# Kernel optimization log

Hardware: AMD Instinct MI355X
Metric: run time of the kernel (lower is better)

Reference implementation:

```python
import jax, jax.numpy as jnp
import numpy as np

B, S, D, H = 2, 2048, 1024, 16
DK = D // H


def setup_inputs() -> dict:
    key = jax.random.key(0)
    ks = jax.random.split(key, 12)
    sc = 0.02
    return {
        "q": jax.random.normal(ks[0], (B, S, D), jnp.float32),
        "k": jax.random.normal(ks[1], (B, S, D), jnp.float32),
        "v": jax.random.normal(ks[2], (B, S, D), jnp.float32),
        "Wq": jax.random.normal(ks[3], (D, D), jnp.float32) * sc,
        "bq": jnp.zeros((D,), jnp.float32),
        "Wk": jax.random.normal(ks[4], (D, D), jnp.float32) * sc,
        "bk": jnp.zeros((D,), jnp.float32),
        "Wv": jax.random.normal(ks[5], (D, D), jnp.float32) * sc,
        "bv": jnp.zeros((D,), jnp.float32),
        "Wo": jax.random.normal(ks[6], (D, D), jnp.float32) * sc,
        "bo": jnp.zeros((D,), jnp.float32),
        "mask": jnp.ones((1, 1, S, S), jnp.int32),
    }


def reference(q, k, v, Wq, bq, Wk, bk, Wv, bv, Wo, bo, mask):
    # Linear projections (torch Linear: x @ W.T + b)
    query = q @ Wq.T + bq  # [B, S, D]
    key_ = k @ Wk.T + bk
    value = v @ Wv.T + bv
    # split heads -> [B, H, S, DK]
    def split(x):
        return x.reshape(B, S, H, DK).transpose(0, 2, 1, 3)
    query, key_, value = split(query), split(key_), split(value)
    scores = jnp.einsum("bhqd,bhkd->bhqk", query, key_) / jnp.sqrt(jnp.float32(DK))
    scores = jnp.where(mask == 0, jnp.float32(-1e9), scores)
    attn = jax.nn.softmax(scores, axis=-1)  # dropout=0.0 -> identity
    out = jnp.einsum("bhqk,bhkd->bhqd", attn, value)  # [B, H, S, DK]
    out = out.transpose(0, 2, 1, 3).reshape(B, S, D)
    return out @ Wo.T + bo
```

## Files before the change

### kernel.cpp

```cpp
#include <hip/hip_runtime.h>

typedef unsigned short u16;
typedef float f32x4 __attribute__((ext_vector_type(4)));
typedef __bf16 bf16x8 __attribute__((ext_vector_type(8)));
typedef short s16x8 __attribute__((ext_vector_type(8)));
typedef short s16x4 __attribute__((ext_vector_type(4)));

#define QSCALE 0.18033688011112042f

__device__ __forceinline__ u16 f2bf(float f) {
    unsigned int u = __builtin_bit_cast(unsigned int, f);
    u += 0x7fffu + ((u >> 16) & 1u);
    return (u16)(u >> 16);
}

__device__ __forceinline__ f32x4 mfma16(s16x8 a, s16x8 b, f32x4 c) {
    return __builtin_amdgcn_mfma_f32_16x16x32_bf16(
        __builtin_bit_cast(bf16x8, a), __builtin_bit_cast(bf16x8, b), c, 0, 0, 0);
}

__device__ __forceinline__ void cp16(const u16* g, u16* l) {
    __builtin_amdgcn_global_load_lds(
        (const __attribute__((address_space(1))) unsigned int*)g,
        (__attribute__((address_space(3))) unsigned int*)l, 16, 0, 0);
}

__global__ __launch_bounds__(256) void k_cvt(
    const float* q, const float* k, const float* v,
    const float* Wq, const float* Wk, const float* Wv, const float* Wo,
    u16* qb, u16* kb, u16* vb, u16* Wqb, u16* Wkb, u16* Wvb, u16* Wob) {
    const float* src;
    u16* dst;
    int count;
    switch (blockIdx.y) {
        case 0: src = q;  dst = qb;  count = 4194304; break;
        case 1: src = k;  dst = kb;  count = 4194304; break;
        case 2: src = v;  dst = vb;  count = 4194304; break;
        case 3: src = Wq; dst = Wqb; count = 1048576; break;
        case 4: src = Wk; dst = Wkb; count = 1048576; break;
        case 5: src = Wv; dst = Wvb; count = 1048576; break;
        default: src = Wo; dst = Wob; count = 1048576; break;
    }
    const int idx = (blockIdx.x * 256 + threadIdx.x) * 8;
    if (idx >= count) return;
    const f32x4 f0 = *(const f32x4*)(src + idx);
    const f32x4 f1 = *(const f32x4*)(src + idx + 4);
    s16x8 o;
#pragma unroll
    for (int i = 0; i < 4; i++) o[i] = (short)f2bf(f0[i]);
#pragma unroll
    for (int i = 0; i < 4; i++) o[4 + i] = (short)f2bf(f1[i]);
    *(s16x8*)(dst + idx) = o;
}

__device__ __forceinline__ void gemm_dev(const u16* __restrict__ A,
                                         const u16* __restrict__ W,
                                         const float* __restrict__ bias,
                                         u16* __restrict__ dstb,
                                         float* __restrict__ dstf,
                                         int mode, float scale) {
    constexpr int K = 1024;
    __shared__ u16 As[128 * 64];
    __shared__ u16 Bs[128 * 64];
    const int tid = threadIdx.x;
    const int wid = tid >> 6, lane = tid & 63;
    const int ln = lane & 15, qd = lane >> 4;
    const int wm = wid >> 1, wn = wid & 1;
    const int m0 = blockIdx.y * 128, n0 = blockIdx.x * 128;
    const int lrow = lane >> 3, lcol = (lane & 7) * 8;

    f32x4 acc[4][4] = {};

    for (int k0 = 0; k0 < K; k0 += 64) {
        __syncthreads();
#pragma unroll
        for (int c = 0; c < 4; c++) {
            const int ch = wid * 4 + c;
            cp16(A + (m0 + ch * 8 + lrow) * K + k0 + lcol, &As[ch * 512]);
            cp16(W + (n0 + ch * 8 + lrow) * K + k0 + lcol, &Bs[ch * 512]);
        }
        __syncthreads();
#pragma unroll
        for (int kk = 0; kk < 64; kk += 32) {
            s16x8 af[4], bf[4];
#pragma unroll
            for (int t = 0; t < 4; t++) {
                af[t] = *(const s16x8*)&As[(wm * 64 + t * 16 + ln) * 64 + kk + qd * 8];
                bf[t] = *(const s16x8*)&Bs[(wn * 64 + t * 16 + ln) * 64 + kk + qd * 8];
            }
#pragma unroll
            for (int tm = 0; tm < 4; tm++)
#pragma unroll
                for (int tn = 0; tn < 4; tn++)
                    acc[tm][tn] = mfma16(af[tm], bf[tn], acc[tm][tn]);
        }
    }

#pragma unroll
    for (int tn = 0; tn < 4; tn++) {
        const int gn = n0 + wn * 64 + tn * 16 + ln;
        const float bv = bias[gn];
        const int h = gn >> 6, dk = gn & 63;
#pragma unroll
        for (int tm = 0; tm < 4; tm++) {
            const int gmb = m0 + wm * 64 + tm * 16 + qd * 4;
            const f32x4 a = acc[tm][tn];
            if (mode == 0) {
                const int b = gmb >> 11;
#pragma unroll
                for (int r = 0; r < 4; r++) {
                    const int s = (gmb + r) & 2047;
                    dstb[(((b * 16 + h) * 2048) + s) * 64 + dk] =
                        f2bf((a[r] + bv) * scale);
                }
            } else if (mode == 2) {
                const int b = gmb >> 11, s = gmb & 2047;
                s16x4 pk;
#pragma unroll
                for (int r = 0; r < 4; r++) pk[r] = (short)f2bf(a[r] + bv);
                *(s16x4*)&dstb[(((b * 16 + h) * 64) + dk) * 2048 + s] = pk;
            } else {
#pragma unroll
                for (int r = 0; r < 4; r++)
                    dstf[(gmb + r) * 1024 + gn] = a[r] + bv;
            }
        }
    }
}

__global__ __launch_bounds__(256, 2) void k_gemm_qkv(
    const u16* qb, const u16* kb, const u16* vb,
    const u16* Wqb, const u16* Wkb, const u16* Wvb,
    const float* bq, const float* bk, const float* bv,
    u16* Qw, u16* Kw, u16* Vt) {
    const int z = blockIdx.z;
    const u16* A = (z == 0) ? qb : (z == 1) ? kb : vb;
    const u16* W = (z == 0) ? Wqb : (z == 1) ? Wkb : Wvb;
    const float* bi = (z == 0) ? bq : (z == 1) ? bk : bv;
    u16* dst = (z == 0) ? Qw : (z == 1) ? Kw : Vt;
    const int mode = (z == 2) ? 2 : 0;
    const float scale = (z == 0) ? QSCALE : 1.0f;
    gemm_dev(A, W, bi, dst, nullptr, mode, scale);
}

__global__ __launch_bounds__(256, 2) void k_gemm_o(const u16* A, const u16* W,
                                                   const float* bias, float* out) {
    gemm_dev(A, W, bias, nullptr, out, 1, 1.0f);
}

__global__ __launch_bounds__(256, 2) void k_attn(const u16* __restrict__ Qw,
                                                 const u16* __restrict__ Kw,
                                                 const u16* __restrict__ Vt,
                                                 u16* __restrict__ AO) {
    __shared__ u16 Ks[128 * 64];
    __shared__ u16 Vs[64 * 128];

    const int i = blockIdx.x;
    const int xcd = i & 7, qq = i >> 3;
    const int bh = xcd * 4 + (qq >> 4);
    const int qblk = qq & 15;
    const int tid = threadIdx.x;
    const int wid = tid >> 6, lane = tid & 63;
    const int ln = lane & 15, qd = lane >> 4;
    const int q0 = qblk * 128 + wid * 32;

    const u16* Qp = Qw + (bh * 2048 + q0 + ln) * 64 + qd * 8;
    const s16x8 qA0 = *(const s16x8*)Qp;
    const s16x8 qA1 = *(const s16x8*)(Qp + 32);
    const s16x8 qB0 = *(const s16x8*)(Qp + 16 * 64);
    const s16x8 qB1 = *(const s16x8*)(Qp + 16 * 64 + 32);

    int Kgoff[4], Vgoff[4];
#pragma unroll
    for (int c = 0; c < 4; c++) {
        const int ch = wid * 4 + c;
        {
            const int kl = ch * 8 + (lane >> 3);
            const int slot = lane & 7;
            const int cK = (slot - 2 * (kl & 7) - (kl >> 3)) & 7;
            Kgoff[c] = (bh * 2048 + kl) * 64 + cK * 8;
        }
        {
            const int d = ch * 4 + (lane >> 4);
            const int slot = lane & 15;
            const int cV = (slot - d) & 15;
            Vgoff[c] = (bh * 64 + d) * 2048 + cV * 8;
        }
    }

    const int kf0 = (ln >> 2) * 8 + (ln & 3);
    const int rotbase = 2 * (ln & 3) + (ln >> 2);

    f32x4 oA[4] = {}, oB[4] = {};
    float lsA = 0.0f, lsB = 0.0f;
    const f32x4 zero = {};

    for (int kb = 0; kb < 2048; kb += 128) {
        __syncthreads();
#pragma unroll
        for (int c = 0; c < 4; c++) {
            cp16(Kw + Kgoff[c] + kb * 64, &Ks[(wid * 4 + c) * 512]);
            cp16(Vt + Vgoff[c] + kb,      &Vs[(wid * 4 + c) * 512]);
        }
        __syncthreads();
#pragma unroll
        for (int sc = 0; sc < 4; sc++) {
            const int rot = (rotbase + sc * 4) & 7;
            const int s0 = (qd + rot) & 7;
            const int kbase = (sc * 32 + kf0) * 64;
            const s16x8 k00 = *(const s16x8*)&Ks[kbase + s0 * 8];
            const s16x8 k01 = *(const s16x8*)&Ks[kbase + (s0 ^ 4) * 8];
            const s16x8 k10 = *(const s16x8*)&Ks[kbase + 256 + s0 * 8];
            const s16x8 k11 = *(const s16x8*)&Ks[kbase + 256 + (s0 ^ 4) * 8];

            f32x4 cA0 = mfma16(k00, qA0, zero); cA0 = mfma16(k01, qA1, cA0);
            f32x4 cA1 = mfma16(k10, qA0, zero); cA1 = mfma16(k11, qA1, cA1);
            f32x4 cB0 = mfma16(k00, qB0, zero); cB0 = mfma16(k01, qB1, cB0);
            f32x4 cB1 = mfma16(k10, qB0, zero); cB1 = mfma16(k11, qB1, cB1);

            bf16x8 pA, pB;
#pragma unroll
            for (int j = 0; j < 4; j++) {
                const float p = __builtin_amdgcn_exp2f(cA0[j]);
                lsA += p; pA[j] = (__bf16)p;
            }
#pragma unroll
            for (int j = 0; j < 4; j++) {
                const float p = __builtin_amdgcn_exp2f(cA1[j]);
                lsA += p; pA[4 + j] = (__bf16)p;
            }
#pragma unroll
            for (int j = 0; j < 4; j++) {
                const float p = __builtin_amdgcn_exp2f(cB0[j]);
                lsB += p; pB[j] = (__bf16)p;
            }
#pragma unroll
            for (int j = 0; j < 4; j++) {
                const float p = __builtin_amdgcn_exp2f(cB1[j]);
                lsB += p; pB[4 + j] = (__bf16)p;
            }
            const s16x8 pAs = __builtin_bit_cast(s16x8, pA);
            const s16x8 pBs = __builtin_bit_cast(s16x8, pB);

            const int vslot = ((sc * 4 + qd + ln) & 15) * 8;
#pragma unroll
            for (int t = 0; t < 4; t++) {
                const s16x8 vf = *(const s16x8*)&Vs[(t * 16 + ln) * 128 + vslot];
                oA[t] = mfma16(vf, pAs, oA[t]);
                oB[t] = mfma16(vf, pBs, oB[t]);
            }
        }
    }

    lsA += __shfl_xor(lsA, 16, 64);
    lsA += __shfl_xor(lsA, 32, 64);
    lsB += __shfl_xor(lsB, 16, 64);
    lsB += __shfl_xor(lsB, 32, 64);
    const float rlA = 1.0f / lsA;
    const float rlB = 1.0f / lsB;

    const int b = bh >> 4, h = bh & 15;
    u16* outA = AO + (b * 2048 + q0 + ln) * 1024 + h * 64;
    u16* outB = outA + 16 * 1024;
#pragma unroll
    for (int t = 0; t < 4; t++)
#pragma unroll
        for (int r = 0; r < 4; r++) {
            const int d = t * 16 + qd * 4 + r;
            outA[d] = f2bf(oA[t][r] * rlA);
            outB[d] = f2bf(oB[t][r] * rlB);
        }
}

extern "C" void kernel_launch(void* const* d_in, const int* in_sizes, int n_in,
                              void* d_out, int out_size, void* d_ws, size_t ws_size,
                              hipStream_t stream) {
    const float* q  = (const float*)d_in[0];
    const float* k  = (const float*)d_in[1];
    const float* v  = (const float*)d_in[2];
    const float* Wq = (const float*)d_in[3];
    const float* bq = (const float*)d_in[4];
    const float* Wk = (const float*)d_in[5];
    const float* bk = (const float*)d_in[6];
    const float* Wv = (const float*)d_in[7];
    const float* bv = (const float*)d_in[8];
    const float* Wo = (const float*)d_in[9];
    const float* bo = (const float*)d_in[10];

    u16* ws = (u16*)d_ws;
    u16* qb  = ws;
    u16* kb  = ws + 4194304;
    u16* vb  = ws + 8388608;
    u16* Wqb = ws + 12582912;
    u16* Wkb = ws + 13631488;
    u16* Wvb = ws + 14680064;
    u16* Wob = ws + 15728640;
    u16* Qw  = ws + 16777216;
    u16* Kw  = ws + 20971520;
    u16* Vt  = ws + 25165824;
    u16* AO  = qb;

    k_cvt<<<dim3(2048, 7), dim3(256), 0, stream>>>(q, k, v, Wq, Wk, Wv, Wo,
                                                   qb, kb, vb, Wqb, Wkb, Wvb, Wob);
    k_gemm_qkv<<<dim3(8, 32, 3), dim3(256), 0, stream>>>(qb, kb, vb, Wqb, Wkb, Wvb,
                                                         bq, bk, bv, Qw, Kw, Vt);
    k_attn<<<dim3(512), dim3(256), 0, stream>>>(Qw, Kw, Vt, AO);
    k_gemm_o<<<dim3(8, 32, 1), dim3(256), 0, stream>>>(AO, Wob, bo, (float*)d_out);
}
```

Measured before the change: 236.6 us.

## Fuse fp32 activation conversion into QKV GEMM and restructure attention wave split

Drops the separate fp32-to-bf16 conversion of q/k/v. The QKV GEMM now loads fp32 activations straight into LDS and converts them to bf16 when building fragments, which removes a full write and re-read of the activations. The attention kernel is reorganised so each wave covers 64 queries over half the keys per tile, reusing each K/V fragment across four query fragments. The two key-halves are then reduced through LDS and written out as coalesced 16-byte stores. In exchange the GEMM doubles its LDS footprint for A tiles, and attention adds extra LDS reduction passes and synchronisation plus higher register pressure.

```diff
diff --git a/kernel.cpp b/kernel.cpp
--- a/kernel.cpp
+++ b/kernel.cpp
@@ -19,30 +19,24 @@
         __builtin_bit_cast(bf16x8, a), __builtin_bit_cast(bf16x8, b), c, 0, 0, 0);
 }
 
-__device__ __forceinline__ void cp16(const u16* g, u16* l) {
+__device__ __forceinline__ void cp16(const void* g, void* l) {
     __builtin_amdgcn_global_load_lds(
         (const __attribute__((address_space(1))) unsigned int*)g,
         (__attribute__((address_space(3))) unsigned int*)l, 16, 0, 0);
 }
 
-__global__ __launch_bounds__(256) void k_cvt(
-    const float* q, const float* k, const float* v,
+__global__ __launch_bounds__(256) void k_cvt_w(
     const float* Wq, const float* Wk, const float* Wv, const float* Wo,
-    u16* qb, u16* kb, u16* vb, u16* Wqb, u16* Wkb, u16* Wvb, u16* Wob) {
+    u16* Wqb, u16* Wkb, u16* Wvb, u16* Wob) {
     const float* src;
     u16* dst;
-    int count;
     switch (blockIdx.y) {
-        case 0: src = q;  dst = qb;  count = 4194304; break;
-        case 1: src = k;  dst = kb;  count = 4194304; break;
-        case 2: src = v;  dst = vb;  count = 4194304; break;
-        case 3: src = Wq; dst = Wqb; count = 1048576; break;
-        case 4: src = Wk; dst = Wkb; count = 1048576; break;
-        case 5: src = Wv; dst = Wvb; count = 1048576; break;
-        default: src = Wo; dst = Wob; count = 1048576; break;
+        case 0: src = Wq; dst = Wqb; break;
+        case 1: src = Wk; dst = Wkb; break;
+        case 2: src = Wv; dst = Wvb; break;
+        default: src = Wo; dst = Wob; break;
     }
     const int idx = (blockIdx.x * 256 + threadIdx.x) * 8;
-    if (idx >= count) return;
     const f32x4 f0 = *(const f32x4*)(src + idx);
     const f32x4 f1 = *(const f32x4*)(src + idx + 4);
     s16x8 o;
@@ -53,15 +47,95 @@
     *(s16x8*)(dst + idx) = o;
 }
 
-__device__ __forceinline__ void gemm_dev(const u16* __restrict__ A,
-                                         const u16* __restrict__ W,
-                                         const float* __restrict__ bias,
-                                         u16* __restrict__ dstb,
-                                         float* __restrict__ dstf,
-                                         int mode, float scale) {
-    constexpr int K = 1024;
-    __shared__ u16 As[128 * 64];
-    __shared__ u16 Bs[128 * 64];
+__global__ __launch_bounds__(256, 2) void k_gemm_qkv(
+    const float* q, const float* k, const float* v,
+    const u16* Wqb, const u16* Wkb, const u16* Wvb,
+    const float* bq, const float* bk, const float* bv,
+    u16* Qw, u16* Kw, u16* Vt) {
+    __shared__ __align__(16) float Asf[128 * 64];
+    __shared__ __align__(16) u16 Ws[128 * 64];
+    const int z = blockIdx.z;
+    const float* A = (z == 0) ? q : (z == 1) ? k : v;
+    const u16* Wb = (z == 0) ? Wqb : (z == 1) ? Wkb : Wvb;
+    const float* bias = (z == 0) ? bq : (z == 1) ? bk : bv;
+    const float scale = (z == 0) ? QSCALE : 1.0f;
+
+    const int tid = threadIdx.x;
+    const int wid = tid >> 6, lane = tid & 63;
+    const int ln = lane & 15, qd = lane >> 4;
+    const int wm = wid >> 1, wn = wid & 1;
+    const int m0 = blockIdx.y * 128, n0 = blockIdx.x * 128;
+
+    f32x4 acc[4][4] = {};
+
+    for (int k0 = 0; k0 < 1024; k0 += 64) {
+        __syncthreads();
+#pragma unroll
+        for (int c = 0; c < 8; c++) {
+            const int ch = wid * 8 + c;
+            cp16(A + (m0 + ch * 4 + (lane >> 4)) * 1024 + k0 + (lane & 15) * 4,
+                 &Asf[ch * 256]);
+        }
+#pragma unroll
+        for (int c = 0; c < 4; c++) {
+            const int ch = wid * 4 + c;
+            cp16(Wb + (n0 + ch * 8 + (lane >> 3)) * 1024 + k0 + (lane & 7) * 8,
+                 &Ws[ch * 512]);
+        }
+        __syncthreads();
+#pragma unroll
+        for (int kk = 0; kk < 64; kk += 32) {
+            s16x8 af[4], bf[4];
+#pragma unroll
+            for (int t = 0; t < 4; t++) {
+                const float* ap = &Asf[(wm * 64 + t * 16 + ln) * 64 + kk + qd * 8];
+                const f32x4 a0 = *(const f32x4*)ap;
+                const f32x4 a1 = *(const f32x4*)(ap + 4);
+                bf16x8 tmp;
+#pragma unroll
+                for (int i = 0; i < 4; i++) { tmp[i] = (__bf16)a0[i]; tmp[4 + i] = (__bf16)a1[i]; }
+                af[t] = __builtin_bit_cast(s16x8, tmp);
+                bf[t] = *(const s16x8*)&Ws[(wn * 64 + t * 16 + ln) * 64 + kk + qd * 8];
+            }
+#pragma unroll
+            for (int tm = 0; tm < 4; tm++)
+#pragma unroll
+                for (int tn = 0; tn < 4; tn++)
+                    acc[tm][tn] = mfma16(af[tm], bf[tn], acc[tm][tn]);
+        }
+    }
+
+#pragma unroll
+    for (int tn = 0; tn < 4; tn++) {
+        const int gn = n0 + wn * 64 + tn * 16 + ln;
+        const float bv2 = bias[gn];
+        const int h = gn >> 6, dk = gn & 63;
+#pragma unroll
+        for (int tm = 0; tm < 4; tm++) {
+            const int gmb = m0 + wm * 64 + tm * 16 + qd * 4;
+            const f32x4 a = acc[tm][tn];
+            const int b = gmb >> 11, s = gmb & 2047;
+            if (z != 2) {
+#pragma unroll
+                for (int r = 0; r < 4; r++)
+                    ((z == 0) ? Qw : Kw)[(((b * 16 + h) * 2048) + s + r) * 64 + dk] =
+                        f2bf((a[r] + bv2) * scale);
+            } else {
+                s16x4 pk;
+#pragma unroll
+                for (int r = 0; r < 4; r++) pk[r] = (short)f2bf(a[r] + bv2);
+                *(s16x4*)&Vt[(((b * 16 + h) * 64) + dk) * 2048 + s] = pk;
+            }
+        }
+    }
+}
+
+__global__ __launch_bounds__(256, 2) void k_gemm_o(const u16* __restrict__ A,
+                                                   const u16* __restrict__ W,
+                                                   const float* __restrict__ bias,
+                                                   float* __restrict__ out) {
+    __shared__ __align__(16) u16 As[128 * 64];
+    __shared__ __align__(16) u16 Bs[128 * 64];
     const int tid = threadIdx.x;
     const int wid = tid >> 6, lane = tid & 63;
     const int ln = lane & 15, qd = lane >> 4;
@@ -70,14 +144,13 @@
     const int lrow = lane >> 3, lcol = (lane & 7) * 8;
 
     f32x4 acc[4][4] = {};
-
-    for (int k0 = 0; k0 < K; k0 += 64) {
+    for (int k0 = 0; k0 < 1024; k0 += 64) {
         __syncthreads();
 #pragma unroll
         for (int c = 0; c < 4; c++) {
             const int ch = wid * 4 + c;
-            cp16(A + (m0 + ch * 8 + lrow) * K + k0 + lcol, &As[ch * 512]);
-            cp16(W + (n0 + ch * 8 + lrow) * K + k0 + lcol, &Bs[ch * 512]);
+            cp16(A + (m0 + ch * 8 + lrow) * 1024 + k0 + lcol, &As[ch * 512]);
+            cp16(W + (n0 + ch * 8 + lrow) * 1024 + k0 + lcol, &Bs[ch * 512]);
         }
         __syncthreads();
 #pragma unroll
@@ -95,65 +168,29 @@
                     acc[tm][tn] = mfma16(af[tm], bf[tn], acc[tm][tn]);
         }
     }
-
 #pragma unroll
     for (int tn = 0; tn < 4; tn++) {
         const int gn = n0 + wn * 64 + tn * 16 + ln;
         const float bv = bias[gn];
-        const int h = gn >> 6, dk = gn & 63;
 #pragma unroll
         for (int tm = 0; tm < 4; tm++) {
             const int gmb = m0 + wm * 64 + tm * 16 + qd * 4;
             const f32x4 a = acc[tm][tn];
-            if (mode == 0) {
-                const int b = gmb >> 11;
-#pragma unroll
-                for (int r = 0; r < 4; r++) {
-                    const int s = (gmb + r) & 2047;
-                    dstb[(((b * 16 + h) * 2048) + s) * 64 + dk] =
-                        f2bf((a[r] + bv) * scale);
-                }
-            } else if (mode == 2) {
-                const int b = gmb >> 11, s = gmb & 2047;
-                s16x4 pk;
-#pragma unroll
-                for (int r = 0; r < 4; r++) pk[r] = (short)f2bf(a[r] + bv);
-                *(s16x4*)&dstb[(((b * 16 + h) * 64) + dk) * 2048 + s] = pk;
-            } else {
-#pragma unroll
-                for (int r = 0; r < 4; r++)
-                    dstf[(gmb + r) * 1024 + gn] = a[r] + bv;
-            }
-        }
-    }
-}
-
-__global__ __launch_bounds__(256, 2) void k_gemm_qkv(
-    const u16* qb, const u16* kb, const u16* vb,
-    const u16* Wqb, const u16* Wkb, const u16* Wvb,
-    const float* bq, const float* bk, const float* bv,
-    u16* Qw, u16* Kw, u16* Vt) {
-    const int z = blockIdx.z;
-    const u16* A = (z == 0) ? qb : (z == 1) ? kb : vb;
-    const u16* W = (z == 0) ? Wqb : (z == 1) ? Wkb : Wvb;
-    const float* bi = (z == 0) ? bq : (z == 1) ? bk : bv;
-    u16* dst = (z == 0) ? Qw : (z == 1) ? Kw : Vt;
-    const int mode = (z == 2) ? 2 : 0;
-    const float scale = (z == 0) ? QSCALE : 1.0f;
-    gemm_dev(A, W, bi, dst, nullptr, mode, scale);
-}
-
-__global__ __launch_bounds__(256, 2) void k_gemm_o(const u16* A, const u16* W,
-                                                   const float* bias, float* out) {
-    gemm_dev(A, W, bias, nullptr, out, 1, 1.0f);
+#pragma unroll
+            for (int r = 0; r < 4; r++) out[(gmb + r) * 1024 + gn] = a[r] + bv;
+        }
+    }
 }
 
 __global__ __launch_bounds__(256, 2) void k_attn(const u16* __restrict__ Qw,
                                                  const u16* __restrict__ Kw,
                                                  const u16* __restrict__ Vt,
                                                  u16* __restrict__ AO) {
-    __shared__ u16 Ks[128 * 64];
-    __shared__ u16 Vs[64 * 128];
+    __shared__ __align__(16) u16 smem[16896];
+    u16* Ks = smem;
+    u16* Vs = smem + 8192;
+    float* Of = (float*)smem;
+    float* Lf = (float*)(smem + 16384);
 
     const int i = blockIdx.x;
     const int xcd = i & 7, qq = i >> 3;
@@ -162,13 +199,16 @@
     const int tid = threadIdx.x;
     const int wid = tid >> 6, lane = tid & 63;
     const int ln = lane & 15, qd = lane >> 4;
-    const int q0 = qblk * 128 + wid * 32;
-
-    const u16* Qp = Qw + (bh * 2048 + q0 + ln) * 64 + qd * 8;
-    const s16x8 qA0 = *(const s16x8*)Qp;
-    const s16x8 qA1 = *(const s16x8*)(Qp + 32);
-    const s16x8 qB0 = *(const s16x8*)(Qp + 16 * 64);
-    const s16x8 qB1 = *(const s16x8*)(Qp + 16 * 64 + 32);
+    const int qg = wid >> 1, kg = wid & 1;
+    const int q0 = qblk * 128;
+
+    const u16* Qp = Qw + (bh * 2048 + q0 + qg * 64 + ln) * 64 + qd * 8;
+    s16x8 qf[4][2];
+#pragma unroll
+    for (int f = 0; f < 4; f++) {
+        qf[f][0] = *(const s16x8*)(Qp + f * 16 * 64);
+        qf[f][1] = *(const s16x8*)(Qp + f * 16 * 64 + 32);
+    }
 
     int Kgoff[4], Vgoff[4];
 #pragma unroll
@@ -191,8 +231,8 @@
     const int kf0 = (ln >> 2) * 8 + (ln & 3);
     const int rotbase = 2 * (ln & 3) + (ln >> 2);
 
-    f32x4 oA[4] = {}, oB[4] = {};
-    float lsA = 0.0f, lsB = 0.0f;
+    f32x4 of[4][4] = {};
+    float lsp[4] = {};
     const f32x4 zero = {};
 
     for (int kb = 0; kb < 2048; kb += 128) {
@@ -204,72 +244,92 @@
         }
         __syncthreads();
 #pragma unroll
-        for (int sc = 0; sc < 4; sc++) {
-            const int rot = (rotbase + sc * 4) & 7;
+        for (int sc = 0; sc < 2; sc++) {
+            const int sp = kg * 2 + sc;
+            const int rot = (rotbase + sp * 4) & 7;
             const int s0 = (qd + rot) & 7;
-            const int kbase = (sc * 32 + kf0) * 64;
+            const int kbase = (sp * 32 + kf0) * 64;
             const s16x8 k00 = *(const s16x8*)&Ks[kbase + s0 * 8];
             const s16x8 k01 = *(const s16x8*)&Ks[kbase + (s0 ^ 4) * 8];
             const s16x8 k10 = *(const s16x8*)&Ks[kbase + 256 + s0 * 8];
             const s16x8 k11 = *(const s16x8*)&Ks[kbase + 256 + (s0 ^ 4) * 8];
 
-            f32x4 cA0 = mfma16(k00, qA0, zero); cA0 = mfma16(k01, qA1, cA0);
-            f32x4 cA1 = mfma16(k10, qA0, zero); cA1 = mfma16(k11, qA1, cA1);
-            f32x4 cB0 = mfma16(k00, qB0, zero); cB0 = mfma16(k01, qB1, cB0);
-            f32x4 cB1 = mfma16(k10, qB0, zero); cB1 = mfma16(k11, qB1, cB1);
-
-            bf16x8 pA, pB;
-#pragma unroll
-            for (int j = 0; j < 4; j++) {
-                const float p = __builtin_amdgcn_exp2f(cA0[j]);
-                lsA += p; pA[j] = (__bf16)p;
-            }
-#pragma unroll
-            for (int j = 0; j < 4; j++) {
-                const float p = __builtin_amdgcn_exp2f(cA1[j]);
-                lsA += p; pA[4 + j] = (__bf16)p;
-            }
-#pragma unroll
-            for (int j = 0; j < 4; j++) {
-                const float p = __builtin_amdgcn_exp2f(cB0[j]);
-                lsB += p; pB[j] = (__bf16)p;
-            }
-#pragma unroll
-            for (int j = 0; j < 4; j++) {
-                const float p = __builtin_amdgcn_exp2f(cB1[j]);
-                lsB += p; pB[4 + j] = (__bf16)p;
-            }
-            const s16x8 pAs = __builtin_bit_cast(s16x8, pA);
-            const s16x8 pBs = __builtin_bit_cast(s16x8, pB);
-
-            const int vslot = ((sc * 4 + qd + ln) & 15) * 8;
+            s16x8 pf[4];
+#pragma unroll
+            for (int f = 0; f < 4; f++) {
+                f32x4 c0 = mfma16(k00, qf[f][0], zero); c0 = mfma16(k01, qf[f][1], c0);
+                f32x4 c1 = mfma16(k10, qf[f][0], zero); c1 = mfma16(k11, qf[f][1], c1);
+                bf16x8 p;
+#pragma unroll
+                for (int j = 0; j < 4; j++) {
+                    const float e = __builtin_amdgcn_exp2f(c0[j]);
+                    lsp[f] += e; p[j] = (__bf16)e;
+                }
+#pragma unroll
+                for (int j = 0; j < 4; j++) {
+                    const float e = __builtin_amdgcn_exp2f(c1[j]);
+                    lsp[f] += e; p[4 + j] = (__bf16)e;
+                }
+                pf[f] = __builtin_bit_cast(s16x8, p);
+            }
+            const int vslot = ((sp * 4 + qd + ln) & 15) * 8;
 #pragma unroll
             for (int t = 0; t < 4; t++) {
                 const s16x8 vf = *(const s16x8*)&Vs[(t * 16 + ln) * 128 + vslot];
-                oA[t] = mfma16(vf, pAs, oA[t]);
-                oB[t] = mfma16(vf, pBs, oB[t]);
-            }
-        }
-    }
-
-    lsA += __shfl_xor(lsA, 16, 64);
-    lsA += __shfl_xor(lsA, 32, 64);
-    lsB += __shfl_xor(lsB, 16, 64);
-    lsB += __shfl_xor(lsB, 32, 64);
-    const float rlA = 1.0f / lsA;
-    const float rlB = 1.0f / lsB;
-
+#pragma unroll
+                for (int f = 0; f < 4; f++)
+                    of[t][f] = mfma16(vf, pf[f], of[t][f]);
+            }
+        }
+    }
+
+#pragma unroll
+    for (int f = 0; f < 4; f++) {
+        lsp[f] += __shfl_xor(lsp[f], 16, 64);
+        lsp[f] += __shfl_xor(lsp[f], 32, 64);
+    }
+    __syncthreads();
+    if (qd == 0) {
+#pragma unroll
+        for (int f = 0; f < 4; f++) Lf[qg * 128 + kg * 64 + f * 16 + ln] = lsp[f];
+    }
+    if (kg == 0) {
+#pragma unroll
+        for (int t = 0; t < 4; t++)
+#pragma unroll
+            for (int f = 0; f < 4; f++)
+#pragma unroll
+                for (int r = 0; r < 4; r++)
+                    Of[qg * 4096 + (t * 16 + qd * 4 + r) * 64 + f * 16 + ln] =
+                        of[t][f][r];
+    }
+    __syncthreads();
+    if (kg == 1) {
+#pragma unroll
+        for (int t = 0; t < 4; t++)
+#pragma unroll
+            for (int f = 0; f < 4; f++)
+#pragma unroll
+                for (int r = 0; r < 4; r++)
+                    Of[qg * 4096 + (t * 16 + qd * 4 + r) * 64 + f * 16 + ln] +=
+                        of[t][f][r];
+    }
+    __syncthreads();
+
+    const int ql = kg * 32 + (lane >> 1);
+    const int d0 = (lane & 1) * 32;
+    const float rl = 1.0f / (Lf[qg * 128 + ql] + Lf[qg * 128 + 64 + ql]);
+    const int qglob = q0 + qg * 64 + ql;
     const int b = bh >> 4, h = bh & 15;
-    u16* outA = AO + (b * 2048 + q0 + ln) * 1024 + h * 64;
-    u16* outB = outA + 16 * 1024;
-#pragma unroll
-    for (int t = 0; t < 4; t++)
-#pragma unroll
-        for (int r = 0; r < 4; r++) {
-            const int d = t * 16 + qd * 4 + r;
-            outA[d] = f2bf(oA[t][r] * rlA);
-            outB[d] = f2bf(oB[t][r] * rlB);
-        }
+    u16* dst = AO + (b * 2048 + qglob) * 1024 + h * 64 + d0;
+#pragma unroll
+    for (int c8 = 0; c8 < 4; c8++) {
+        s16x8 ov;
+#pragma unroll
+        for (int j = 0; j < 8; j++)
+            ov[j] = (short)f2bf(Of[qg * 4096 + (d0 + c8 * 8 + j) * 64 + ql] * rl);
+        *(s16x8*)(dst + c8 * 8) = ov;
+    }
 }
 
 extern "C" void kernel_launch(void* const* d_in, const int* in_sizes, int n_in,
@@ -288,21 +348,18 @@
     const float* bo = (const float*)d_in[10];
 
     u16* ws = (u16*)d_ws;
-    u16* qb  = ws;
-    u16* kb  = ws + 4194304;
-    u16* vb  = ws + 8388608;
-    u16* Wqb = ws + 12582912;
-    u16* Wkb = ws + 13631488;
-    u16* Wvb = ws + 14680064;
-    u16* Wob = ws + 15728640;
-    u16* Qw  = ws + 16777216;
-    u16* Kw  = ws + 20971520;
-    u16* Vt  = ws + 25165824;
-    u16* AO  = qb;
-
-    k_cvt<<<dim3(2048, 7), dim3(256), 0, stream>>>(q, k, v, Wq, Wk, Wv, Wo,
-                                                   qb, kb, vb, Wqb, Wkb, Wvb, Wob);
-    k_gemm_qkv<<<dim3(8, 32, 3), dim3(256), 0, stream>>>(qb, kb, vb, Wqb, Wkb, Wvb,
+    u16* Wqb = ws;
+    u16* Wkb = ws + 1048576;
+    u16* Wvb = ws + 2097152;
+    u16* Wob = ws + 3145728;
+    u16* Qw  = ws + 4194304;
+    u16* Kw  = ws + 8388608;
+    u16* Vt  = ws + 12582912;
+    u16* AO  = ws + 16777216;
+
+    k_cvt_w<<<dim3(512, 4), dim3(256), 0, stream>>>(Wq, Wk, Wv, Wo,
+                                                    Wqb, Wkb, Wvb, Wob);
+    k_gemm_qkv<<<dim3(8, 32, 3), dim3(256), 0, stream>>>(q, k, v, Wqb, Wkb, Wvb,
                                                          bq, bk, bv, Qw, Kw, Vt);
     k_attn<<<dim3(512), dim3(256), 0, stream>>>(Qw, Kw, Vt, AO);
     k_gemm_o<<<dim3(8, 32, 1), dim3(256), 0, stream>>>(AO, Wob, bo, (float*)d_out);
```

New measurement: 247.8 us. 4.7% more time.

## Split attention key range across wave pairs, swizzle GEMM LDS, vectorize output

Applied to the files above, without the earlier changes.

Attention waves are regrouped so that two waves share 64 queries and each handles half of every 128-key tile. Each K/V fragment read from LDS then feeds four query fragments instead of two. The partial outputs and row sums of the two halves are combined through shared memory at the end, and the result is written as 16-byte vectorized rows. The GEMM LDS tiles get a rotation swizzle to reduce bank conflicts on fragment reads. In exchange, each wave holds more accumulator registers, which may lower occupancy, and the final reduction adds extra shared-memory passes and barriers.

```diff
diff --git a/kernel.cpp b/kernel.cpp
--- a/kernel.cpp
+++ b/kernel.cpp
@@ -19,7 +19,7 @@
         __builtin_bit_cast(bf16x8, a), __builtin_bit_cast(bf16x8, b), c, 0, 0, 0);
 }
 
-__device__ __forceinline__ void cp16(const u16* g, u16* l) {
+__device__ __forceinline__ void cp16(const void* g, void* l) {
     __builtin_amdgcn_global_load_lds(
         (const __attribute__((address_space(1))) unsigned int*)g,
         (__attribute__((address_space(3))) unsigned int*)l, 16, 0, 0);
@@ -60,14 +60,15 @@
                                          float* __restrict__ dstf,
                                          int mode, float scale) {
     constexpr int K = 1024;
-    __shared__ u16 As[128 * 64];
-    __shared__ u16 Bs[128 * 64];
+    __shared__ __align__(16) u16 As[128 * 64];
+    __shared__ __align__(16) u16 Bs[128 * 64];
     const int tid = threadIdx.x;
     const int wid = tid >> 6, lane = tid & 63;
     const int ln = lane & 15, qd = lane >> 4;
     const int wm = wid >> 1, wn = wid & 1;
     const int m0 = blockIdx.y * 128, n0 = blockIdx.x * 128;
-    const int lrow = lane >> 3, lcol = (lane & 7) * 8;
+    const int lrow = lane >> 3;
+    const int scol = (((lane & 7) - (lane >> 3)) & 7) * 8;
 
     f32x4 acc[4][4] = {};
 
@@ -76,17 +77,18 @@
 #pragma unroll
         for (int c = 0; c < 4; c++) {
             const int ch = wid * 4 + c;
-            cp16(A + (m0 + ch * 8 + lrow) * K + k0 + lcol, &As[ch * 512]);
-            cp16(W + (n0 + ch * 8 + lrow) * K + k0 + lcol, &Bs[ch * 512]);
+            cp16(A + (m0 + ch * 8 + lrow) * K + k0 + scol, &As[ch * 512]);
+            cp16(W + (n0 + ch * 8 + lrow) * K + k0 + scol, &Bs[ch * 512]);
         }
         __syncthreads();
 #pragma unroll
         for (int kk = 0; kk < 64; kk += 32) {
+            const int sA = ((qd + (kk >> 3) + ln) & 7) * 8;
             s16x8 af[4], bf[4];
 #pragma unroll
             for (int t = 0; t < 4; t++) {
-                af[t] = *(const s16x8*)&As[(wm * 64 + t * 16 + ln) * 64 + kk + qd * 8];
-                bf[t] = *(const s16x8*)&Bs[(wn * 64 + t * 16 + ln) * 64 + kk + qd * 8];
+                af[t] = *(const s16x8*)&As[(wm * 64 + t * 16 + ln) * 64 + sA];
+                bf[t] = *(const s16x8*)&Bs[(wn * 64 + t * 16 + ln) * 64 + sA];
             }
 #pragma unroll
             for (int tm = 0; tm < 4; tm++)
@@ -105,16 +107,13 @@
         for (int tm = 0; tm < 4; tm++) {
             const int gmb = m0 + wm * 64 + tm * 16 + qd * 4;
             const f32x4 a = acc[tm][tn];
+            const int b = gmb >> 11, s = gmb & 2047;
             if (mode == 0) {
-                const int b = gmb >> 11;
-#pragma unroll
-                for (int r = 0; r < 4; r++) {
-                    const int s = (gmb + r) & 2047;
-                    dstb[(((b * 16 + h) * 2048) + s) * 64 + dk] =
+#pragma unroll
+                for (int r = 0; r < 4; r++)
+                    dstb[(((b * 16 + h) * 2048) + s + r) * 64 + dk] =
                         f2bf((a[r] + bv) * scale);
-                }
             } else if (mode == 2) {
-                const int b = gmb >> 11, s = gmb & 2047;
                 s16x4 pk;
 #pragma unroll
                 for (int r = 0; r < 4; r++) pk[r] = (short)f2bf(a[r] + bv);
@@ -152,8 +151,11 @@
                                                  const u16* __restrict__ Kw,
                                                  const u16* __restrict__ Vt,
                                                  u16* __restrict__ AO) {
-    __shared__ u16 Ks[128 * 64];
-    __shared__ u16 Vs[64 * 128];
+    __shared__ __align__(16) u16 smem[16896];
+    u16* Ks = smem;
+    u16* Vs = smem + 8192;
+    float* Of = (float*)smem;
+    float* Lf = (float*)(smem + 16384);
 
     const int i = blockIdx.x;
     const int xcd = i & 7, qq = i >> 3;
@@ -162,13 +164,16 @@
     const int tid = threadIdx.x;
     const int wid = tid >> 6, lane = tid & 63;
     const int ln = lane & 15, qd = lane >> 4;
-    const int q0 = qblk * 128 + wid * 32;
-
-    const u16* Qp = Qw + (bh * 2048 + q0 + ln) * 64 + qd * 8;
-    const s16x8 qA0 = *(const s16x8*)Qp;
-    const s16x8 qA1 = *(const s16x8*)(Qp + 32);
-    const s16x8 qB0 = *(const s16x8*)(Qp + 16 * 64);
-    const s16x8 qB1 = *(const s16x8*)(Qp + 16 * 64 + 32);
+    const int qg = wid >> 1, kg = wid & 1;
+    const int q0 = qblk * 128;
+
+    const u16* Qp = Qw + (bh * 2048 + q0 + qg * 64 + ln) * 64 + qd * 8;
+    s16x8 qf[4][2];
+#pragma unroll
+    for (int f = 0; f < 4; f++) {
+        qf[f][0] = *(const s16x8*)(Qp + f * 16 * 64);
+        qf[f][1] = *(const s16x8*)(Qp + f * 16 * 64 + 32);
+    }
 
     int Kgoff[4], Vgoff[4];
 #pragma unroll
@@ -191,8 +196,8 @@
     const int kf0 = (ln >> 2) * 8 + (ln & 3);
     const int rotbase = 2 * (ln & 3) + (ln >> 2);
 
-    f32x4 oA[4] = {}, oB[4] = {};
-    float lsA = 0.0f, lsB = 0.0f;
+    f32x4 of[4][4] = {};
+    float lsp[4] = {};
     const f32x4 zero = {};
 
     for (int kb = 0; kb < 2048; kb += 128) {
@@ -204,72 +209,92 @@
         }
         __syncthreads();
 #pragma unroll
-        for (int sc = 0; sc < 4; sc++) {
-            const int rot = (rotbase + sc * 4) & 7;
+        for (int sc = 0; sc < 2; sc++) {
+            const int sp = kg * 2 + sc;
+            const int rot = (rotbase + sp * 4) & 7;
             const int s0 = (qd + rot) & 7;
-            const int kbase = (sc * 32 + kf0) * 64;
+            const int kbase = (sp * 32 + kf0) * 64;
             const s16x8 k00 = *(const s16x8*)&Ks[kbase + s0 * 8];
             const s16x8 k01 = *(const s16x8*)&Ks[kbase + (s0 ^ 4) * 8];
             const s16x8 k10 = *(const s16x8*)&Ks[kbase + 256 + s0 * 8];
             const s16x8 k11 = *(const s16x8*)&Ks[kbase + 256 + (s0 ^ 4) * 8];
 
-            f32x4 cA0 = mfma16(k00, qA0, zero); cA0 = mfma16(k01, qA1, cA0);
-            f32x4 cA1 = mfma16(k10, qA0, zero); cA1 = mfma16(k11, qA1, cA1);
-            f32x4 cB0 = mfma16(k00, qB0, zero); cB0 = mfma16(k01, qB1, cB0);
-            f32x4 cB1 = mfma16(k10, qB0, zero); cB1 = mfma16(k11, qB1, cB1);
-
-            bf16x8 pA, pB;
-#pragma unroll
-            for (int j = 0; j < 4; j++) {
-                const float p = __builtin_amdgcn_exp2f(cA0[j]);
-                lsA += p; pA[j] = (__bf16)p;
+            s16x8 pf[4];
+#pragma unroll
+            for (int f = 0; f < 4; f++) {
+                f32x4 c0 = mfma16(k00, qf[f][0], zero); c0 = mfma16(k01, qf[f][1], c0);
+                f32x4 c1 = mfma16(k10, qf[f][0], zero); c1 = mfma16(k11, qf[f][1], c1);
+                bf16x8 p;
+#pragma unroll
+                for (int j = 0; j < 4; j++) {
+                    const float e = __builtin_amdgcn_exp2f(c0[j]);
+                    lsp[f] += e; p[j] = (__bf16)e;
+                }
+#pragma unroll
+                for (int j = 0; j < 4; j++) {
+                    const float e = __builtin_amdgcn_exp2f(c1[j]);
+                    lsp[f] += e; p[4 + j] = (__bf16)e;
+                }
+                pf[f] = __builtin_bit_cast(s16x8, p);
             }
-#pragma unroll
-            for (int j = 0; j < 4; j++) {
-                const float p = __builtin_amdgcn_exp2f(cA1[j]);
-                lsA += p; pA[4 + j] = (__bf16)p;
-            }
-#pragma unroll
-            for (int j = 0; j < 4; j++) {
-                const float p = __builtin_amdgcn_exp2f(cB0[j]);
-                lsB += p; pB[j] = (__bf16)p;
-            }
-#pragma unroll
-            for (int j = 0; j < 4; j++) {
-                const float p = __builtin_amdgcn_exp2f(cB1[j]);
-                lsB += p; pB[4 + j] = (__bf16)p;
-            }
-            const s16x8 pAs = __builtin_bit_cast(s16x8, pA);
-            const s16x8 pBs = __builtin_bit_cast(s16x8, pB);
-
-            const int vslot = ((sc * 4 + qd + ln) & 15) * 8;
+            const int vslot = ((sp * 4 + qd + ln) & 15) * 8;
 #pragma unroll
             for (int t = 0; t < 4; t++) {
                 const s16x8 vf = *(const s16x8*)&Vs[(t * 16 + ln) * 128 + vslot];
-                oA[t] = mfma16(vf, pAs, oA[t]);
-                oB[t] = mfma16(vf, pBs, oB[t]);
+#pragma unroll
+                for (int f = 0; f < 4; f++)
+                    of[t][f] = mfma16(vf, pf[f], of[t][f]);
             }
         }
     }
 
-    lsA += __shfl_xor(lsA, 16, 64);
-    lsA += __shfl_xor(lsA, 32, 64);
-    lsB += __shfl_xor(lsB, 16, 64);
-    lsB += __shfl_xor(lsB, 32, 64);
-    const float rlA = 1.0f / lsA;
-    const float rlB = 1.0f / lsB;
-
+#pragma unroll
+    for (int f = 0; f < 4; f++) {
+        lsp[f] += __shfl_xor(lsp[f], 16, 64);
+        lsp[f] += __shfl_xor(lsp[f], 32, 64);
+    }
+    __syncthreads();
+    if (qd == 0) {
+#pragma unroll
+        for (int f = 0; f < 4; f++) Lf[qg * 128 + kg * 64 + f * 16 + ln] = lsp[f];
+    }
+    if (kg == 0) {
+#pragma unroll
+        for (int t = 0; t < 4; t++)
+#pragma unroll
+            for (int f = 0; f < 4; f++)
+#pragma unroll
+                for (int r = 0; r < 4; r++)
+                    Of[qg * 4096 + (t * 16 + qd * 4 + r) * 64 + f * 16 + ln] =
+                        of[t][f][r];
+    }
+    __syncthreads();
+    if (kg == 1) {
+#pragma unroll
+        for (int t = 0; t < 4; t++)
+#pragma unroll
+            for (int f = 0; f < 4; f++)
+#pragma unroll
+                for (int r = 0; r < 4; r++)
+                    Of[qg * 4096 + (t * 16 + qd * 4 + r) * 64 + f * 16 + ln] +=
+                        of[t][f][r];
+    }
+    __syncthreads();
+
+    const int ql = kg * 32 + (lane >> 1);
+    const int d0 = (lane & 1) * 32;
+    const float rl = 1.0f / (Lf[qg * 128 + ql] + Lf[qg * 128 + 64 + ql]);
+    const int qglob = q0 + qg * 64 + ql;
     const int b = bh >> 4, h = bh & 15;
-    u16* outA = AO + (b * 2048 + q0 + ln) * 1024 + h * 64;
-    u16* outB = outA + 16 * 1024;
-#pragma unroll
-    for (int t = 0; t < 4; t++)
-#pragma unroll
-        for (int r = 0; r < 4; r++) {
-            const int d = t * 16 + qd * 4 + r;
-            outA[d] = f2bf(oA[t][r] * rlA);
-            outB[d] = f2bf(oB[t][r] * rlB);
-        }
+    u16* dst = AO + (b * 2048 + qglob) * 1024 + h * 64 + d0;
+#pragma unroll
+    for (int c8 = 0; c8 < 4; c8++) {
+        s16x8 ov;
+#pragma unroll
+        for (int j = 0; j < 8; j++)
+            ov[j] = (short)f2bf(Of[qg * 4096 + (d0 + c8 * 8 + j) * 64 + ql] * rl);
+        *(s16x8*)(dst + c8 * 8) = ov;
+    }
 }
 
 extern "C" void kernel_launch(void* const* d_in, const int* in_sizes, int n_in,
```

After: 226.4 us. -4.3%, faster.
